# Kernel tuning notes

Measured on AMD Instinct MI355X. Metric: run time of the kernel, lower is better.

The kernel has to match this reference:

```python
import jax, jax.numpy as jnp
import numpy as np

BSZ, T, H, P, N = 2, 2048, 16, 64, 64

def setup_inputs() -> dict:
    key = jax.random.key(0)
    k1, k2, k3, k4, k5 = jax.random.split(key, 5)
    X = jax.random.normal(k1, (BSZ, T, H, P), dtype=jnp.float32)
    delta = jax.random.uniform(k2, (BSZ, T, H), dtype=jnp.float32)
    Bmat = jax.random.normal(k3, (BSZ, T, N), dtype=jnp.float32)
    Cmat = jax.random.normal(k4, (BSZ, T, N), dtype=jnp.float32)
    # module init: A_log = log(arange(1, n_heads+1))
    A_log = jnp.log(jnp.arange(1, H + 1, dtype=jnp.float32))
    return {"X": X, "delta": delta, "Bmat": Bmat, "Cmat": Cmat, "A_log": A_log}

def reference(X, delta, Bmat, Cmat, A_log):
    # X: [B,T,H,P], delta: [B,T,H], Bmat/Cmat: [B,T,N], A_log: [H]
    Bsz, Tlen, Hh, Pp = X.shape
    Nn = Bmat.shape[-1]
    dA = jnp.exp(delta * -jnp.exp(A_log))  # [B,T,H] per-step scalar decay

    def step(h, inp):
        dA_t, dt_t, X_t, B_t, C_t = inp  # [B,H], [B,H], [B,H,P], [B,N], [B,N]
        # outer-product input: delta * X outer B -> [B,H,P,N]
        dBx = (dt_t[:, :, None, None] * X_t[..., None]) * B_t[:, None, None, :]
        h = dA_t[:, :, None, None] * h + dBx
        y_t = jnp.einsum('bhpn,bn->bhp', h, C_t)
        return h, y_t

    h0 = jnp.zeros((Bsz, Hh, Pp, Nn), dtype=X.dtype)
    xs = (
        jnp.moveaxis(dA, 1, 0),    # [T,B,H]
        jnp.moveaxis(delta, 1, 0), # [T,B,H]
        jnp.moveaxis(X, 1, 0),     # [T,B,H,P]
        jnp.moveaxis(Bmat, 1, 0),  # [T,B,N]
        jnp.moveaxis(Cmat, 1, 0),  # [T,B,N]
    )
    h_last, ys = jax.lax.scan(step, h0, xs)
    y = jnp.moveaxis(ys, 0, 1)  # [B,T,H,P]
    return y, h_last
```

## Files before the change

### kernel.cpp

```cpp
#include <hip/hip_runtime.h>


constexpr int BSZ = 2, T = 2048, H = 16, P = 64, N = 64;
constexpr int L = 64, NC = T / L;
constexpr int LSB = 72;

using bf16x8 = __attribute__((ext_vector_type(8))) short;
using f32x4  = __attribute__((ext_vector_type(4))) float;

__device__ inline ushort f2bf(float f) {
    unsigned u = __float_as_uint(f);
    u += 0x7FFFu + ((u >> 16) & 1u);
    return (ushort)(u >> 16);
}
__device__ inline unsigned pack2(float a, float b) {
    return (unsigned)f2bf(a) | ((unsigned)f2bf(b) << 16);
}
__device__ inline float bf2f(ushort h) {
    return __uint_as_float(((unsigned)h) << 16);
}
__device__ inline int swz(int row, int col) {
    return row * 64 + ((((col >> 3) ^ (row & 7))) << 3) + (col & 7);
}

typedef __attribute__((address_space(3))) unsigned int       lds_u32;
typedef const __attribute__((address_space(1))) unsigned int glb_u32;
__device__ inline void dma16(const void* g, void* l) {
    __builtin_amdgcn_global_load_lds((glb_u32*)g, (lds_u32*)l, 16, 0, 0);
}
__device__ inline void dma4(const void* g, void* l) {
    __builtin_amdgcn_global_load_lds((glb_u32*)g, (lds_u32*)l, 4, 0, 0);
}

__global__ __launch_bounds__(256, 4) void ka_prep(
    const float* __restrict__ X, const float* __restrict__ delta,
    const float* __restrict__ Bm, const float* __restrict__ Cm,
    const float* __restrict__ A_log,
    ushort* __restrict__ Xtg, ushort* __restrict__ Hbuf,
    ushort* __restrict__ Bbf, ushort* __restrict__ Cbf,
    float* __restrict__ Vec, float* __restrict__ Dchunk)
{
    __shared__ __align__(16) ushort sXt[4096];
    __shared__ __align__(16) ushort sBt[64 * LSB];
    __shared__ float sWf[64];

    const int tid  = threadIdx.x, lane = tid & 63, w = tid >> 6;
    const int quad = lane >> 4,   l16  = lane & 15;
    const int blk = blockIdx.x;
    const int h   = blk & (H - 1);
    const int c   = (blk >> 4) & (NC - 1);
    const int b   = blk >> 9;
    const int t0  = c * L;
    const int chunkid = (b * H + h) * NC + c;
    const int bcid    = b * NC + c;

    {
        const float* gB = Bm + ((size_t)b * T + t0) * N;
        #pragma unroll
        for (int i = 0; i < 8; ++i) {
            int tau = (w * 8 + i) * 2;
            *(unsigned*)&sBt[lane * LSB + tau] =
                pack2(gB[(size_t)tau * N + lane], gB[(size_t)(tau + 1) * N + lane]);
        }
    }
    {
        const float* gX = X + (((size_t)b * T + t0) * H + h) * P;
        #pragma unroll
        for (int i = 0; i < 8; ++i) {
            int tau = w * 16 + 2 * i;
            *(unsigned*)&sXt[swz(lane, tau)] =
                pack2(gX[(size_t)tau * (H * P) + lane],
                      gX[(size_t)(tau + 1) * (H * P) + lane]);
        }
    }
    if (h == 0) {
        const float4* gB4 = (const float4*)(Bm + ((size_t)b * T + t0) * N);
        const float4* gC4 = (const float4*)(Cm + ((size_t)b * T + t0) * N);
        ushort* Bt = Bbf + (size_t)bcid * 4096;
        ushort* Ct = Cbf + (size_t)bcid * 4096;
        #pragma unroll
        for (int r = 0; r < 4; ++r) {
            int idx = r * 256 + tid, t = idx >> 4, n4 = idx & 15;
            int g = n4 >> 1, half = n4 & 1;
            int off = t * 64 + (((g ^ (t & 7))) << 3) + half * 4;
            float4 vb = gB4[idx], vc = gC4[idx];
            *(uint2*)&Bt[off] = make_uint2(pack2(vb.x, vb.y), pack2(vb.z, vb.w));
            *(uint2*)&Ct[off] = make_uint2(pack2(vc.x, vc.y), pack2(vc.z, vc.w));
        }
    }
    if (w == 0) {
        float dl = delta[((size_t)b * T + t0 + lane) * H + h];
        float s = -__expf(A_log[h]) * dl;
        #pragma unroll
        for (int off = 1; off < 64; off <<= 1) {
            float u = __shfl_up(s, off, 64);
            if (lane >= off) s += u;
        }
        float sL  = __shfl(s, 63, 64);
        float lnd = __logf(dl);
        sWf[lane] = __expf(sL + lnd - s);
        float* vp = Vec + (size_t)chunkid * 192;
        vp[lane]       = s;
        vp[64 + lane]  = lnd - s;
        vp[128 + lane] = __expf(s);
        if (lane == 63) Dchunk[chunkid] = __expf(sL);
    }
    __syncthreads();

    f32x4 ha[4];
    #pragma unroll
    for (int j = 0; j < 4; ++j) ha[j] = (f32x4){0.f, 0.f, 0.f, 0.f};
    #pragma unroll
    for (int ks = 0; ks < 2; ++ks) {
        const int ko = ks * 32 + quad * 8;
        const int sg = (ko >> 3) ^ (l16 & 7);
        bf16x8 xa = *(const bf16x8*)&sXt[(w * 16 + l16) * 64 + sg * 8];
        union { bf16x8 v; unsigned u[4]; } xw;
        #pragma unroll
        for (int j2 = 0; j2 < 4; ++j2)
            xw.u[j2] = pack2(bf2f((ushort)xa[2*j2])   * sWf[ko + 2*j2],
                             bf2f((ushort)xa[2*j2+1]) * sWf[ko + 2*j2+1]);
        #pragma unroll
        for (int jn = 0; jn < 4; ++jn) {
            bf16x8 bb = *(const bf16x8*)&sBt[(jn * 16 + l16) * LSB + ko];
            ha[jn] = __builtin_amdgcn_mfma_f32_16x16x32_bf16(xw.v, bb, ha[jn], 0, 0, 0);
        }
    }

    {
        ushort* Xtt = Xtg + (size_t)chunkid * 4096;
        #pragma unroll
        for (int i = 0; i < 2; ++i) {
            int j = i * 256 + tid;
            ((uint4*)Xtt)[j] = ((const uint4*)sXt)[j];
        }
    }
    __syncthreads();
    {
        ushort* hst = sBt;
        #pragma unroll
        for (int jn = 0; jn < 4; ++jn)
            #pragma unroll
            for (int r = 0; r < 4; ++r)
                hst[swz(w * 16 + quad * 4 + r, jn * 16 + l16)] = f2bf(ha[jn][r]);
    }
    __syncthreads();
    {
        ushort* Ht = Hbuf + (size_t)chunkid * 4096;
        #pragma unroll
        for (int i = 0; i < 2; ++i) {
            int j = i * 256 + tid;
            ((uint4*)Ht)[j] = ((const uint4*)sBt)[j];
        }
    }
}

__global__ __launch_bounds__(256, 4) void k2_scan(
    const float* __restrict__ Dchunk, ushort* __restrict__ Hbuf,
    float* __restrict__ Hlast)
{
    const unsigned gid = blockIdx.x * 256u + threadIdx.x;
    const int bh  = gid >> 11;
    const int rem = gid & 2047;
    unsigned* Hb = (unsigned*)Hbuf;
    unsigned v[NC];
    #pragma unroll
    for (int cc = 0; cc < NC; ++cc)
        v[cc] = Hb[(size_t)(bh * NC + cc) * 2048 + rem];
    float hx = 0.f, hy = 0.f;
    #pragma unroll
    for (int cc = 0; cc < NC; ++cc) {
        const float lo = bf2f((ushort)(v[cc] & 0xffffu));
        const float hi = bf2f((ushort)(v[cc] >> 16));
        v[cc] = pack2(hx, hy);
        const float D = Dchunk[bh * NC + cc];
        hx = D * hx + lo;
        hy = D * hy + hi;
    }
    #pragma unroll
    for (int cc = 0; cc < NC; ++cc)
        Hb[(size_t)(bh * NC + cc) * 2048 + rem] = v[cc];
    const int p   = rem >> 5, w32 = rem & 31;
    const int g   = (w32 >> 2) ^ (p & 7);
    const int n0  = (g << 3) + ((w32 & 3) << 1);
    *(float2*)&Hlast[(size_t)bh * 4096 + p * 64 + n0] = make_float2(hx, hy);
}

__global__ __launch_bounds__(256, 4) void k3_y(
    const ushort* __restrict__ Xtg, const ushort* __restrict__ Bbf,
    const ushort* __restrict__ Cbf, const float* __restrict__ Vec,
    const ushort* __restrict__ Hbuf, float* __restrict__ Y)
{
    __shared__ __align__(16) ushort sC [4096];
    __shared__ __align__(16) ushort sB [4096];
    __shared__ __align__(16) ushort sXt[4096];
    __shared__ __align__(16) ushort sH [4096];
    __shared__ float sVec[192];

    const int tid  = threadIdx.x, lane = tid & 63, w = tid >> 6;
    const int quad = lane >> 4,   l16  = lane & 15;
    const int blk = blockIdx.x;
    const int h   = blk & (H - 1);
    const int c   = (blk >> 4) & (NC - 1);
    const int b   = blk >> 9;
    const int t0  = c * L;
    const int chunkid = (b * H + h) * NC + c;
    const int bcid    = b * NC + c;

    {
        const ushort* gsrc;
        ushort* ldst;
        if      (w == 0) { gsrc = Cbf + (size_t)bcid * 4096;    ldst = sC;  }
        else if (w == 1) { gsrc = Bbf + (size_t)bcid * 4096;    ldst = sB;  }
        else if (w == 2) { gsrc = Xtg + (size_t)chunkid * 4096; ldst = sXt; }
        else             { gsrc = Hbuf + (size_t)chunkid * 4096; ldst = sH; }
        const char* g = (const char*)gsrc + lane * 16;
        #pragma unroll
        for (int i = 0; i < 8; ++i)
            dma16(g + i * 1024, (char*)ldst + i * 1024);
        if (w == 0) {
            const float* vp = Vec + (size_t)chunkid * 192;
            dma4(vp + lane,       sVec);
            dma4(vp + 64 + lane,  sVec + 64);
            dma4(vp + 128 + lane, sVec + 128);
        }
    }
    __syncthreads();

    f32x4 g4[4];
    #pragma unroll
    for (int j = 0; j < 4; ++j) g4[j] = (f32x4){0.f, 0.f, 0.f, 0.f};
    #pragma unroll
    for (int ks = 0; ks < 2; ++ks) {
        const int ko = ks * 32 + quad * 8;
        const int sg = (ko >> 3) ^ (l16 & 7);
        bf16x8 af = *(const bf16x8*)&sC[(w * 16 + l16) * 64 + sg * 8];
        #pragma unroll
        for (int jt = 0; jt < 4; ++jt) {
            bf16x8 bfr = *(const bf16x8*)&sB[(jt * 16 + l16) * 64 + sg * 8];
            g4[jt] = __builtin_amdgcn_mfma_f32_16x16x32_bf16(af, bfr, g4[jt], 0, 0, 0);
        }
    }
    __syncthreads();

    #pragma unroll
    for (int jt = 0; jt < 4; ++jt) {
        const int tau = jt * 16 + l16;
        const float sbv = sVec[64 + tau];
        #pragma unroll
        for (int r = 0; r < 4; ++r) {
            const int t = w * 16 + quad * 4 + r;
            float arg = (tau <= t) ? (sVec[t] + sbv) : -80.0f;
            sB[swz(t, tau)] = f2bf(__expf(arg) * g4[jt][r]);
        }
    }
    __syncthreads();

    f32x4 ya[4], acc[4];
    #pragma unroll
    for (int j = 0; j < 4; ++j) {
        ya[j]  = (f32x4){0.f, 0.f, 0.f, 0.f};
        acc[j] = (f32x4){0.f, 0.f, 0.f, 0.f};
    }
    #pragma unroll
    for (int ks = 0; ks < 2; ++ks) {
        const int ko = ks * 32 + quad * 8;
        const int sg = (ko >> 3) ^ (l16 & 7);
        bf16x8 sa = *(const bf16x8*)&sB[(w * 16 + l16) * 64 + sg * 8];
        bf16x8 ca = *(const bf16x8*)&sC[(w * 16 + l16) * 64 + sg * 8];
        #pragma unroll
        for (int jp = 0; jp < 4; ++jp) {
            bf16x8 xb = *(const bf16x8*)&sXt[(jp * 16 + l16) * 64 + sg * 8];
            bf16x8 hb = *(const bf16x8*)&sH [(jp * 16 + l16) * 64 + sg * 8];
            ya[jp]  = __builtin_amdgcn_mfma_f32_16x16x32_bf16(sa, xb, ya[jp], 0, 0, 0);
            acc[jp] = __builtin_amdgcn_mfma_f32_16x16x32_bf16(ca, hb, acc[jp], 0, 0, 0);
        }
    }

    float* Yg = Y + (((size_t)b * T + t0) * H + h) * P;
    #pragma unroll
    for (int jp = 0; jp < 4; ++jp)
        #pragma unroll
        for (int r = 0; r < 4; ++r) {
            const int t = w * 16 + quad * 4 + r;
            Yg[(size_t)t * (H * P) + jp * 16 + l16] =
                ya[jp][r] + sVec[128 + t] * acc[jp][r];
        }
}

extern "C" void kernel_launch(void* const* d_in, const int* in_sizes, int n_in,
                              void* d_out, int out_size, void* d_ws, size_t ws_size,
                              hipStream_t stream) {
    const float* X     = (const float*)d_in[0];
    const float* delta = (const float*)d_in[1];
    const float* Bm    = (const float*)d_in[2];
    const float* Cm    = (const float*)d_in[3];
    const float* A_log = (const float*)d_in[4];

    float* Y     = (float*)d_out;
    float* Hlast = (float*)d_out + (size_t)BSZ * T * H * P;

    char* ws = (char*)d_ws;
    ushort* Hbuf = (ushort*)(ws);
    ushort* Xtg  = (ushort*)(ws + (8u << 20));
    ushort* Bbf  = (ushort*)(ws + (16u << 20));
    ushort* Cbf  = (ushort*)(ws + (16u << 20) + (512u << 10));
    float*  Vec  = (float*)(ws + (17u << 20));
    float*  Dchunk = (float*)(ws + (18u << 20));

    const int nblk = BSZ * NC * H;
    ka_prep<<<nblk, 256, 0, stream>>>(X, delta, Bm, Cm, A_log,
                                      Xtg, Hbuf, Bbf, Cbf, Vec, Dchunk);
    k2_scan<<<256, 256, 0, stream>>>(Dchunk, Hbuf, Hlast);
    k3_y<<<nblk, 256, 0, stream>>>(Xtg, Bbf, Cbf, Vec, Hbuf, Y);
}
```

Before: 96.85 us.

## Fuse three SSD kernels into one cooperative kernel with grid barriers

Replaces the prep, inter-chunk scan and output kernels with a single cooperative kernel that uses two software grid barriers built on atomics. Intermediate data such as X, B and decay vectors stay in LDS instead of going through global workspace, and two kernel launch gaps disappear. In exchange it adds an extra memset, barrier spin costs, and the scan phase runs only on wave 0 of each block. It falls back to the three-kernel path if the cooperative launch fails.

```diff
diff --git a/kernel.cpp b/kernel.cpp
--- a/kernel.cpp
+++ b/kernel.cpp
@@ -3,6 +3,7 @@
 
 constexpr int BSZ = 2, T = 2048, H = 16, P = 64, N = 64;
 constexpr int L = 64, NC = T / L;
+constexpr int NBLK = BSZ * NC * H;
 constexpr int LSB = 72;
 
 using bf16x8 = __attribute__((ext_vector_type(8))) short;
@@ -30,6 +31,249 @@
 }
 __device__ inline void dma4(const void* g, void* l) {
     __builtin_amdgcn_global_load_lds((glb_u32*)g, (lds_u32*)l, 4, 0, 0);
+}
+
+__device__ inline void grid_sync(unsigned* cnt, unsigned* gate) {
+    __syncthreads();
+    if (threadIdx.x == 0) {
+        __threadfence();
+        unsigned arrived = __hip_atomic_fetch_add(
+            cnt, 1u, __ATOMIC_ACQ_REL, __HIP_MEMORY_SCOPE_AGENT) + 1u;
+        if (arrived == (unsigned)NBLK) {
+            __hip_atomic_store(gate, 1u, __ATOMIC_RELEASE,
+                               __HIP_MEMORY_SCOPE_AGENT);
+        } else {
+            while (__hip_atomic_load(gate, __ATOMIC_ACQUIRE,
+                                     __HIP_MEMORY_SCOPE_AGENT) == 0u)
+                __builtin_amdgcn_s_sleep(2);
+        }
+        __threadfence();
+    }
+    __syncthreads();
+}
+
+__global__ __launch_bounds__(256, 4) void fused_ssd(
+    const float* __restrict__ X, const float* __restrict__ delta,
+    const float* __restrict__ Bm, const float* __restrict__ Cm,
+    const float* __restrict__ A_log,
+    ushort* __restrict__ Hbuf, float* __restrict__ Dchunk,
+    float* __restrict__ Y, float* __restrict__ Hlast,
+    unsigned* __restrict__ bar)
+{
+    __shared__ __align__(16) ushort sXt[4096];
+    __shared__ __align__(16) ushort sB [4096];
+    __shared__ __align__(16) ushort sH [4096];
+    __shared__ float sVec[256];
+
+    const int tid  = threadIdx.x, lane = tid & 63, w = tid >> 6;
+    const int quad = lane >> 4,   l16  = lane & 15;
+    const int blk = blockIdx.x;
+    const int h   = blk & (H - 1);
+    const int c   = (blk >> 4) & (NC - 1);
+    const int b   = blk >> 9;
+    const int t0  = c * L;
+    const int chunkid = (b * H + h) * NC + c;
+
+    {
+        const float* gB = Bm + ((size_t)b * T + t0) * N;
+        #pragma unroll
+        for (int i = 0; i < 8; ++i) {
+            int tau = (w * 8 + i) * 2;
+            *(unsigned*)&sH[swz(lane, tau)] =
+                pack2(gB[(size_t)tau * N + lane], gB[(size_t)(tau + 1) * N + lane]);
+        }
+    }
+    {
+        const float* gX = X + (((size_t)b * T + t0) * H + h) * P;
+        #pragma unroll
+        for (int i = 0; i < 8; ++i) {
+            int tau = w * 16 + 2 * i;
+            *(unsigned*)&sXt[swz(lane, tau)] =
+                pack2(gX[(size_t)tau * (H * P) + lane],
+                      gX[(size_t)(tau + 1) * (H * P) + lane]);
+        }
+    }
+    {
+        const float4* gB4 = (const float4*)(Bm + ((size_t)b * T + t0) * N);
+        #pragma unroll
+        for (int r = 0; r < 4; ++r) {
+            int idx = r * 256 + tid, t = idx >> 4, n4 = idx & 15;
+            int g = n4 >> 1, half = n4 & 1;
+            int off = t * 64 + (((g ^ (t & 7))) << 3) + half * 4;
+            float4 vb = gB4[idx];
+            *(uint2*)&sB[off] = make_uint2(pack2(vb.x, vb.y), pack2(vb.z, vb.w));
+        }
+    }
+    if (w == 0) {
+        float dl = delta[((size_t)b * T + t0 + lane) * H + h];
+        float s = -__expf(A_log[h]) * dl;
+        #pragma unroll
+        for (int off = 1; off < 64; off <<= 1) {
+            float u = __shfl_up(s, off, 64);
+            if (lane >= off) s += u;
+        }
+        float sL  = __shfl(s, 63, 64);
+        float lnd = __logf(dl);
+        sVec[192 + lane] = __expf(sL + lnd - s);
+        sVec[lane]       = s;
+        sVec[64 + lane]  = lnd - s;
+        sVec[128 + lane] = __expf(s);
+        if (lane == 63) Dchunk[chunkid] = __expf(sL);
+    }
+    __syncthreads();
+
+    f32x4 ha[4];
+    #pragma unroll
+    for (int j = 0; j < 4; ++j) ha[j] = (f32x4){0.f, 0.f, 0.f, 0.f};
+    #pragma unroll
+    for (int ks = 0; ks < 2; ++ks) {
+        const int ko = ks * 32 + quad * 8;
+        const int sg = (ko >> 3) ^ (l16 & 7);
+        bf16x8 xa = *(const bf16x8*)&sXt[(w * 16 + l16) * 64 + sg * 8];
+        union { bf16x8 v; unsigned u[4]; } xw;
+        #pragma unroll
+        for (int j2 = 0; j2 < 4; ++j2)
+            xw.u[j2] = pack2(bf2f((ushort)xa[2*j2])   * sVec[192 + ko + 2*j2],
+                             bf2f((ushort)xa[2*j2+1]) * sVec[192 + ko + 2*j2+1]);
+        #pragma unroll
+        for (int jn = 0; jn < 4; ++jn) {
+            bf16x8 bb = *(const bf16x8*)&sH[(jn * 16 + l16) * 64 + sg * 8];
+            ha[jn] = __builtin_amdgcn_mfma_f32_16x16x32_bf16(xw.v, bb, ha[jn], 0, 0, 0);
+        }
+    }
+    __syncthreads();
+    {
+        #pragma unroll
+        for (int jn = 0; jn < 4; ++jn)
+            #pragma unroll
+            for (int r = 0; r < 4; ++r)
+                sH[swz(w * 16 + quad * 4 + r, jn * 16 + l16)] = f2bf(ha[jn][r]);
+    }
+    __syncthreads();
+    {
+        ushort* Ht = Hbuf + (size_t)chunkid * 4096;
+        #pragma unroll
+        for (int i = 0; i < 2; ++i) {
+            int j = i * 256 + tid;
+            ((uint4*)Ht)[j] = ((const uint4*)sH)[j];
+        }
+    }
+
+    grid_sync(bar + 0, bar + 1);
+
+    if (w == 0) {
+        const unsigned gid = blockIdx.x * 64u + lane;
+        const int bh  = gid >> 11;
+        const int rem = gid & 2047;
+        unsigned* Hb = (unsigned*)Hbuf;
+        const float* Dp = Dchunk + bh * NC;
+        float hx = 0.f, hy = 0.f;
+        #pragma unroll
+        for (int half = 0; half < 2; ++half) {
+            unsigned v[16];
+            #pragma unroll
+            for (int i = 0; i < 16; ++i)
+                v[i] = Hb[(size_t)(bh * NC + half * 16 + i) * 2048 + rem];
+            #pragma unroll
+            for (int i = 0; i < 16; ++i) {
+                const float lo = bf2f((ushort)(v[i] & 0xffffu));
+                const float hi = bf2f((ushort)(v[i] >> 16));
+                v[i] = pack2(hx, hy);
+                const float D = Dp[half * 16 + i];
+                hx = D * hx + lo;
+                hy = D * hy + hi;
+            }
+            #pragma unroll
+            for (int i = 0; i < 16; ++i)
+                Hb[(size_t)(bh * NC + half * 16 + i) * 2048 + rem] = v[i];
+        }
+        const int p   = rem >> 5, w32 = rem & 31;
+        const int g   = (w32 >> 2) ^ (p & 7);
+        const int n0  = (g << 3) + ((w32 & 3) << 1);
+        *(float2*)&Hlast[(size_t)bh * 4096 + p * 64 + n0] = make_float2(hx, hy);
+    }
+
+    grid_sync(bar + 2, bar + 3);
+
+    {
+        const char* gsrc = (const char*)(Hbuf + (size_t)chunkid * 4096)
+                           + w * 2048 + lane * 16;
+        char* ldst = (char*)sH + w * 2048;
+        dma16(gsrc, ldst);
+        dma16(gsrc + 1024, ldst + 1024);
+    }
+    bf16x8 cfrag[2];
+    {
+        const float* gC = Cm + ((size_t)b * T + t0 + w * 16 + l16) * N + quad * 8;
+        #pragma unroll
+        for (int ks = 0; ks < 2; ++ks) {
+            float4 c0 = *(const float4*)&gC[ks * 32];
+            float4 c1 = *(const float4*)&gC[ks * 32 + 4];
+            union { bf16x8 v; unsigned u[4]; } cf;
+            cf.u[0] = pack2(c0.x, c0.y); cf.u[1] = pack2(c0.z, c0.w);
+            cf.u[2] = pack2(c1.x, c1.y); cf.u[3] = pack2(c1.z, c1.w);
+            cfrag[ks] = cf.v;
+        }
+    }
+    __syncthreads();
+
+    f32x4 g4[4];
+    #pragma unroll
+    for (int j = 0; j < 4; ++j) g4[j] = (f32x4){0.f, 0.f, 0.f, 0.f};
+    #pragma unroll
+    for (int ks = 0; ks < 2; ++ks) {
+        const int ko = ks * 32 + quad * 8;
+        const int sg = (ko >> 3) ^ (l16 & 7);
+        #pragma unroll
+        for (int jt = 0; jt < 4; ++jt) {
+            bf16x8 bfr = *(const bf16x8*)&sB[(jt * 16 + l16) * 64 + sg * 8];
+            g4[jt] = __builtin_amdgcn_mfma_f32_16x16x32_bf16(cfrag[ks], bfr, g4[jt], 0, 0, 0);
+        }
+    }
+    __syncthreads();
+
+    #pragma unroll
+    for (int jt = 0; jt < 4; ++jt) {
+        const int tau = jt * 16 + l16;
+        const float sbv = sVec[64 + tau];
+        #pragma unroll
+        for (int r = 0; r < 4; ++r) {
+            const int t = w * 16 + quad * 4 + r;
+            float arg = (tau <= t) ? (sVec[t] + sbv) : -80.0f;
+            sB[swz(t, tau)] = f2bf(__expf(arg) * g4[jt][r]);
+        }
+    }
+    __syncthreads();
+
+    f32x4 ya[4], acc[4];
+    #pragma unroll
+    for (int j = 0; j < 4; ++j) {
+        ya[j]  = (f32x4){0.f, 0.f, 0.f, 0.f};
+        acc[j] = (f32x4){0.f, 0.f, 0.f, 0.f};
+    }
+    #pragma unroll
+    for (int ks = 0; ks < 2; ++ks) {
+        const int ko = ks * 32 + quad * 8;
+        const int sg = (ko >> 3) ^ (l16 & 7);
+        bf16x8 sa = *(const bf16x8*)&sB[(w * 16 + l16) * 64 + sg * 8];
+        #pragma unroll
+        for (int jp = 0; jp < 4; ++jp) {
+            bf16x8 xb = *(const bf16x8*)&sXt[(jp * 16 + l16) * 64 + sg * 8];
+            bf16x8 hb = *(const bf16x8*)&sH [(jp * 16 + l16) * 64 + sg * 8];
+            ya[jp]  = __builtin_amdgcn_mfma_f32_16x16x32_bf16(sa, xb, ya[jp], 0, 0, 0);
+            acc[jp] = __builtin_amdgcn_mfma_f32_16x16x32_bf16(cfrag[ks], hb, acc[jp], 0, 0, 0);
+        }
+    }
+
+    float* Yg = Y + (((size_t)b * T + t0) * H + h) * P;
+    #pragma unroll
+    for (int jp = 0; jp < 4; ++jp)
+        #pragma unroll
+        for (int r = 0; r < 4; ++r) {
+            const int t = w * 16 + quad * 4 + r;
+            Yg[(size_t)t * (H * P) + jp * 16 + l16] =
+                ya[jp][r] + sVec[128 + t] * acc[jp][r];
+        }
 }
 
 __global__ __launch_bounds__(256, 4) void ka_prep(
@@ -126,7 +370,6 @@
             ha[jn] = __builtin_amdgcn_mfma_f32_16x16x32_bf16(xw.v, bb, ha[jn], 0, 0, 0);
         }
     }
-
     {
         ushort* Xtt = Xtg + (size_t)chunkid * 4096;
         #pragma unroll
@@ -301,16 +544,26 @@
     float* Hlast = (float*)d_out + (size_t)BSZ * T * H * P;
 
     char* ws = (char*)d_ws;
-    ushort* Hbuf = (ushort*)(ws);
-    ushort* Xtg  = (ushort*)(ws + (8u << 20));
-    ushort* Bbf  = (ushort*)(ws + (16u << 20));
-    ushort* Cbf  = (ushort*)(ws + (16u << 20) + (512u << 10));
-    float*  Vec  = (float*)(ws + (17u << 20));
-    float*  Dchunk = (float*)(ws + (18u << 20));
-
-    const int nblk = BSZ * NC * H;
-    ka_prep<<<nblk, 256, 0, stream>>>(X, delta, Bm, Cm, A_log,
-                                      Xtg, Hbuf, Bbf, Cbf, Vec, Dchunk);
-    k2_scan<<<256, 256, 0, stream>>>(Dchunk, Hbuf, Hlast);
-    k3_y<<<nblk, 256, 0, stream>>>(Xtg, Bbf, Cbf, Vec, Hbuf, Y);
-}
+    unsigned* bar  = (unsigned*)ws;
+    float*  Dchunk = (float*)(ws + 256);
+    ushort* Hbuf   = (ushort*)(ws + (1u << 13));
+    ushort* Xtg    = (ushort*)(ws + (16u << 20));
+    ushort* Bbf    = (ushort*)(ws + (24u << 20));
+    ushort* Cbf    = (ushort*)(ws + (24u << 20) + (512u << 10));
+    float*  Vec    = (float*)(ws + (25u << 20));
+
+    hipMemsetAsync(bar, 0, 64, stream);
+
+    void* args[] = {(void*)&X, (void*)&delta, (void*)&Bm, (void*)&Cm,
+                    (void*)&A_log, (void*)&Hbuf, (void*)&Dchunk,
+                    (void*)&Y, (void*)&Hlast, (void*)&bar};
+    hipError_t e = hipLaunchCooperativeKernel((void*)fused_ssd, dim3(NBLK),
+                                              dim3(256), args, 0, stream);
+    if (e != hipSuccess) {
+        (void)hipGetLastError();
+        ka_prep<<<NBLK, 256, 0, stream>>>(X, delta, Bm, Cm, A_log,
+                                          Xtg, Hbuf, Bbf, Cbf, Vec, Dchunk);
+        k2_scan<<<256, 256, 0, stream>>>(Dchunk, Hbuf, Hlast);
+        k3_y<<<NBLK, 256, 0, stream>>>(Xtg, Bbf, Cbf, Vec, Hbuf, Y);
+    }
+}
```

New measurement: 342.7 us. 3.54x slower.
